# Kernel tuning notes

Measured on AMD Instinct MI355X. Metric: run time of the kernel, lower is better.

The kernel has to match this reference:

```python
import jax, jax.numpy as jnp
import numpy as np

REF_POSE = np.array([[213.33335876464844, 124.50563049316406], [190.504638671875, 115.11840057373047], [169.9791717529297, 101.77180480957031], [146.72341918945312, 96.25749206542969], [128.86770629882812, 87.2344970703125], [150.34292602539062, 101.61070251464844], [119.29926300048828, 98.73982238769531], [100.03463745117188, 99.74459838867188], [82.62400817871094, 101.2509536743164], [148.91049194335938, 112.71517181396484], [114.37303161621094, 113.20121002197266], [91.90096282958984, 116.49812316894531], [74.75020599365234, 119.37875366210938], [149.59658813476562, 124.09295654296875], [119.72419738769531, 126.36898040771484], [99.59107208251953, 129.40196228027344], [82.82524108886719, 131.584228515625], [154.55911254882812, 135.07681274414062], [133.8833770751953, 140.85983276367188], [120.45906066894531, 145.40306091308594], [106.21541595458984, 150.072265625]], dtype=np.float32)

SCALES = (0.25, 0.5, 1.0)
ORIENTATIONS = (0, 90, 180, 270)
INPUT_SIZE = (256, 256)          # (H, W)
ANCHOR_STRIDE = (1, 1)           # (y_stride, x_stride)
POS_TH = 0.5
KPT_SIGMA = 0.05                 # per-keypoint OKS falloff


def _generate_anchor_poses():
    # scale + rotate ref pose about its centroid -> [A, 21, 2]
    c = REF_POSE.mean(axis=0, keepdims=True)
    out = []
    for s in SCALES:
        for o in ORIENTATIONS:
            th = np.deg2rad(o)
            R = np.array([[np.cos(th), -np.sin(th)], [np.sin(th), np.cos(th)]], dtype=np.float32)
            out.append(c + s * (REF_POSE - c) @ R.T)
    return np.stack(out).astype(np.float32)


def _all_anchors(feat_h, feat_w):
    base = _generate_anchor_poses()                      # [A,21,2]
    w_ratio = INPUT_SIZE[1] / feat_w
    h_ratio = INPUT_SIZE[0] / feat_h
    sx = np.arange(0, feat_w, ANCHOR_STRIDE[1]) * w_ratio
    sy = np.arange(0, feat_h, ANCHOR_STRIDE[0]) * h_ratio
    gx, gy = np.meshgrid(sx, sy)
    shifts = np.stack([gx.ravel(), gy.ravel()], axis=1).astype(np.float32)  # [K,2]
    all_a = base[None, :, :, :] + shifts[:, None, None, :]                  # [K,A,21,2]
    return jnp.asarray(all_a.reshape(-1, 21, 2))                            # [K*A,21,2]


def _pose_oks(anchors, gt):
    # anchors [N,21,2], gt [B,2,21,3] -> OKS sim [B,N,2]
    d2 = jnp.sum((anchors[None, :, None, :, :] - gt[:, None, :, :, :2]) ** 2, axis=-1)  # [B,N,2,21]
    vis = (gt[..., 2] > 0).astype(anchors.dtype)[:, None, :, :]                          # [B,1,2,21]
    xy = gt[..., :2]
    area = jnp.prod(xy.max(axis=2) - xy.min(axis=2), axis=-1)                            # [B,2]
    s2 = jnp.maximum(area, 1.0)[:, None, :, None]                                        # [B,1,2,1]
    k2 = (2.0 * KPT_SIGMA) ** 2
    oks = jnp.exp(-d2 / (2.0 * s2 * k2))
    return jnp.sum(oks * vis, axis=-1) / jnp.maximum(jnp.sum(vis, axis=-1), 1.0)          # [B,N,2]


def setup_inputs() -> dict:
    key = jax.random.key(0)
    k1, k2 = jax.random.split(key)
    B = 16
    xy = jax.random.uniform(k1, (B, 42, 2), dtype=jnp.float32) * 216.0 + 20.0
    vis = jnp.ones((B, 42, 1), dtype=jnp.float32)
    pose_gt = jnp.concatenate([xy, vis], axis=-1)          # [B,42,3]
    hand_type = jnp.ones((B, 2), dtype=jnp.int32)          # both hands present
    return {"pose_gt": pose_gt, "hand_type": hand_type, "feat_h": 64, "feat_w": 64}


def reference(pose_gt, hand_type, feat_h, feat_w):
    all_anchors = _all_anchors(feat_h, feat_w)             # [N,21,2], N=K*A
    inside = jnp.sum((all_anchors[..., 0] >= 0) & (all_anchors[..., 1] >= 0)
                     & (all_anchors[..., 0] < INPUT_SIZE[0])
                     & (all_anchors[..., 1] < INPUT_SIZE[1]), axis=1) == 21  # [N]

    B = pose_gt.shape[0]
    gt = pose_gt.reshape(B, 2, 21, 3)                      # hand 0 = right, hand 1 = left
    sim = _pose_oks(all_anchors, gt)                       # [B,N,2]
    am = jnp.argmax(sim, axis=-1)                          # [B,N]
    mx = jnp.max(sim, axis=-1)                             # [B,N]

    right = (am == 0) & (mx > POS_TH) & (hand_type[:, 0:1] == 1) & inside[None, :]
    left = (am == 1) & (mx > POS_TH) & (hand_type[:, 1:2] == 1) & inside[None, :]
    neg = (~right) & (~left) & inside[None, :]

    # labels channel layout matches source: [:,:,0]=left, [:,:,1]=negative, [:,:,2]=right
    labels = jnp.stack([left, neg, right], axis=-1).astype(pose_gt.dtype)   # [B,N,3]
    labels = jnp.where(inside[None, :, None], labels, jnp.asarray(-1.0, pose_gt.dtype))

    pose_targets = (jnp.where(right[..., None, None], gt[:, 0][:, None], 0.0)
                    + jnp.where(left[..., None, None], gt[:, 1][:, None], 0.0))  # [B,N,21,3]

    offsets = pose_targets[..., :2] - all_anchors[None, :, :, :]             # [B,N,21,2]
    offsets = jnp.where(inside[None, :, None, None], offsets, 0.0)
    return all_anchors, inside, labels, offsets
```

## Files before the change

### kernel.cpp

```cpp
#include <hip/hip_runtime.h>
#include <math.h>

#define NA 49152
#define NB 16
#define ABLOCKS 192
#define EPS 1e-3f

__constant__ float RP[21][2] = {
  {213.33335876464844f, 124.50563049316406f},
  {190.504638671875f,   115.11840057373047f},
  {169.9791717529297f,  101.77180480957031f},
  {146.72341918945312f, 96.25749206542969f},
  {128.86770629882812f, 87.2344970703125f},
  {150.34292602539062f, 101.61070251464844f},
  {119.29926300048828f, 98.73982238769531f},
  {100.03463745117188f, 99.74459838867188f},
  {82.62400817871094f,  101.2509536743164f},
  {148.91049194335938f, 112.71517181396484f},
  {114.37303161621094f, 113.20121002197266f},
  {91.90096282958984f,  116.49812316894531f},
  {74.75020599365234f,  119.37875366210938f},
  {149.59658813476562f, 124.09295654296875f},
  {119.72419738769531f, 126.36898040771484f},
  {99.59107208251953f,  129.40196228027344f},
  {82.82524108886719f,  131.584228515625f},
  {154.55911254882812f, 135.07681274414062f},
  {133.8833770751953f,  140.85983276367188f},
  {120.45906066894531f, 145.40306091308594f},
  {106.21541595458984f, 150.072265625f}
};

__device__ __forceinline__ void ref_center(float& cx, float& cy) {
  #pragma clang fp contract(off)
  float rx[8], ry[8];
  #pragma unroll
  for (int j = 0; j < 8; ++j) {
    rx[j] = RP[j][0] + RP[j + 8][0];
    ry[j] = RP[j][1] + RP[j + 8][1];
  }
  float sx = ((rx[0] + rx[1]) + (rx[2] + rx[3])) + ((rx[4] + rx[5]) + (rx[6] + rx[7]));
  float sy = ((ry[0] + ry[1]) + (ry[2] + ry[3])) + ((ry[4] + ry[5]) + (ry[6] + ry[7]));
  #pragma unroll
  for (int j = 16; j < 21; ++j) { sx += RP[j][0]; sy += RP[j][1]; }
  cx = sx / 21.0f;
  cy = sy / 21.0f;
}

__device__ __forceinline__ float2 base_pt(int p, int j, float cx, float cy) {
  #pragma clang fp contract(off)
  const int si = p >> 2, oi = p & 3;
  const float s = (si == 0) ? 0.25f : (si == 1 ? 0.5f : 1.0f);
  const float dx = s * (RP[j][0] - cx);
  const float dy = s * (RP[j][1] - cy);
  const float rx = (oi == 0) ? dx : (oi == 1 ? -dy : (oi == 2 ? -dx : dy));
  const float ry = (oi == 0) ? dy : (oi == 1 ? dx : (oi == 2 ? -dy : -dx));
  return make_float2(cx + rx, cy + ry);
}

__device__ __forceinline__ void dec_anchor(int f2, int a0, const float2* sb2,
                                           float& anx, float& any,
                                           int& aloc, int& j) {
  #pragma clang fp contract(off)
  aloc = f2 / 21;
  j = f2 - aloc * 21;
  const int a = a0 + aloc;
  const int p = a % 12;
  const int kc = a / 12;
  const float shx = 4.0f * (float)(kc & 63);
  const float shy = 4.0f * (float)(kc >> 6);
  const float2 bpv = sb2[p * 21 + j];
  anx = bpv.x + shx;
  any = bpv.y + shy;
}

__device__ __forceinline__ float4 off_quad(int idx, int a0, const float2* sb2,
                                           const float* sgt, const int* shsel) {
  #pragma clang fp contract(off)
  float r[4];
  #pragma unroll
  for (int h = 0; h < 2; ++h) {
    float anx, any; int aloc, j;
    dec_anchor(idx * 2 + h, a0, sb2, anx, any, aloc, j);
    const int cc = shsel[aloc];
    const bool has = (cc == 1) || (cc == 2);
    const int hoff = (cc == 2) ? 63 : 0;
    const float tx = has ? sgt[hoff + j * 3] : 0.0f;
    const float ty = has ? sgt[hoff + j * 3 + 1] : 0.0f;
    r[h * 2]     = (cc >= 0) ? (tx - anx) : 0.0f;
    r[h * 2 + 1] = (cc >= 0) ? (ty - any) : 0.0f;
  }
  return make_float4(r[0], r[1], r[2], r[3]);
}

__device__ __forceinline__ float4 anc_quad(int idx, int a0, const float2* sb2) {
  float r[4];
  #pragma unroll
  for (int h = 0; h < 2; ++h) {
    float anx, any; int aloc, j;
    dec_anchor(idx * 2 + h, a0, sb2, anx, any, aloc, j);
    r[h * 2] = anx;
    r[h * 2 + 1] = any;
  }
  return make_float4(r[0], r[1], r[2], r[3]);
}

__global__ __launch_bounds__(256) void k_all(const float* __restrict__ gt,
                                             const int* __restrict__ ht,
                                             float* __restrict__ oa,
                                             float* __restrict__ oins,
                                             float* __restrict__ ol,
                                             float* __restrict__ oo) {
  __shared__ float2 sb2[252];
  __shared__ float sgt[126];
  __shared__ float sden[2], srden[2], snv[2];
  __shared__ int sht[2];
  __shared__ int shsel[256];
  __shared__ float sins[256];

  const int tid = threadIdx.x;
  const int b = blockIdx.x / ABLOCKS;
  const int ab = blockIdx.x % ABLOCKS;
  const int a0 = ab * 256;

  if (tid < 126) sgt[tid] = gt[b * 126 + tid];
  if (tid < 252) {
    float cx, cy; ref_center(cx, cy);
    const int p = tid / 21;
    const int j = tid - p * 21;
    sb2[tid] = base_pt(p, j, cx, cy);
  }
  if (tid == 252 || tid == 253) {
    const int h = tid - 252;
    const float* g = gt + b * 126 + h * 63;
    float mnx = g[0], mxx = g[0], mny = g[1], mxy = g[1];
    float nv = (g[2] > 0.0f) ? 1.0f : 0.0f;
    for (int j = 1; j < 21; ++j) {
      float x = g[j * 3], y = g[j * 3 + 1];
      mnx = fminf(mnx, x); mxx = fmaxf(mxx, x);
      mny = fminf(mny, y); mxy = fmaxf(mxy, y);
      nv += (g[j * 3 + 2] > 0.0f) ? 1.0f : 0.0f;
    }
    const float area = (mxx - mnx) * (mxy - mny);
    const float s2 = fmaxf(area, 1.0f);
    const float den = (2.0f * s2) * 0.01f;
    sden[h] = den;
    srden[h] = -1.0f / den;
    snv[h] = fmaxf(nv, 1.0f);
  }
  if (tid == 254 || tid == 255) sht[tid - 254] = ht[b * 2 + (tid - 254)];
  __syncthreads();

  const int a = a0 + tid;
  const int p = a % 12;
  const int kc = a / 12;
  const float shx = 4.0f * (float)(kc & 63);
  const float shy = 4.0f * (float)(kc >> 6);
  const float2* bp = sb2 + p * 21;

  const float rd0 = srden[0], rd1 = srden[1];
  bool inside = true;
  float s0f = 0.0f, s1f = 0.0f;
  #pragma unroll
  for (int j = 0; j < 21; ++j) {
    #pragma clang fp contract(off)
    const float anx = bp[j].x + shx;
    const float any = bp[j].y + shy;
    inside = inside && (anx >= 0.0f) && (any >= 0.0f) &&
                       (anx < 256.0f) && (any < 256.0f);
    const float dx0 = anx - sgt[j * 3],      dy0 = any - sgt[j * 3 + 1];
    const float dx1 = anx - sgt[63 + j * 3], dy1 = any - sgt[63 + j * 3 + 1];
    const float v0 = (sgt[j * 3 + 2] > 0.0f) ? 1.0f : 0.0f;
    const float v1 = (sgt[63 + j * 3 + 2] > 0.0f) ? 1.0f : 0.0f;
    s0f += __expf((dx0 * dx0 + dy0 * dy0) * rd0) * v0;
    s1f += __expf((dx1 * dx1 + dy1 * dy1) * rd1) * v1;
  }
  float sim0 = s0f / snv[0];
  float sim1 = s1f / snv[1];
  const float mxf = fmaxf(sim0, sim1);
  const bool need_exact = (fabsf(mxf - 0.5f) < EPS) ||
                          ((mxf > 0.5f - EPS) && (fabsf(sim0 - sim1) < EPS));

  if (need_exact) {
    #pragma clang fp contract(off)
    float q0[8], q1[8];
    #pragma unroll
    for (int j = 0; j < 16; ++j) {
      const float ax = bp[j].x + shx, ay = bp[j].y + shy;
      float dx0 = ax - sgt[j * 3], dy0 = ay - sgt[j * 3 + 1];
      float d20 = dx0 * dx0 + dy0 * dy0;
      float vv0 = (sgt[j * 3 + 2] > 0.0f) ? 1.0f : 0.0f;
      float t0 = (float)::exp((double)(-d20 / sden[0])) * vv0;
      float dx1 = ax - sgt[63 + j * 3], dy1 = ay - sgt[63 + j * 3 + 1];
      float d21 = dx1 * dx1 + dy1 * dy1;
      float vv1 = (sgt[63 + j * 3 + 2] > 0.0f) ? 1.0f : 0.0f;
      float t1 = (float)::exp((double)(-d21 / sden[1])) * vv1;
      if (j < 8) { q0[j] = t0; q1[j] = t1; }
      else       { q0[j - 8] += t0; q1[j - 8] += t1; }
    }
    float s0 = ((q0[0] + q0[1]) + (q0[2] + q0[3])) + ((q0[4] + q0[5]) + (q0[6] + q0[7]));
    float s1 = ((q1[0] + q1[1]) + (q1[2] + q1[3])) + ((q1[4] + q1[5]) + (q1[6] + q1[7]));
    #pragma unroll
    for (int j = 16; j < 21; ++j) {
      const float ax = bp[j].x + shx, ay = bp[j].y + shy;
      float dx0 = ax - sgt[j * 3], dy0 = ay - sgt[j * 3 + 1];
      float d20 = dx0 * dx0 + dy0 * dy0;
      float vv0 = (sgt[j * 3 + 2] > 0.0f) ? 1.0f : 0.0f;
      s0 += (float)::exp((double)(-d20 / sden[0])) * vv0;
      float dx1 = ax - sgt[63 + j * 3], dy1 = ay - sgt[63 + j * 3 + 1];
      float d21 = dx1 * dx1 + dy1 * dy1;
      float vv1 = (sgt[63 + j * 3 + 2] > 0.0f) ? 1.0f : 0.0f;
      s1 += (float)::exp((double)(-d21 / sden[1])) * vv1;
    }
    sim0 = s0 / snv[0];
    sim1 = s1 / snv[1];
  }

  const int am = (sim1 > sim0) ? 1 : 0;
  const float mx = fmaxf(sim0, sim1);
  const bool pos = mx > 0.5f;
  const bool right = (am == 0) && pos && (sht[0] == 1) && inside;
  const bool left  = (am == 1) && pos && (sht[1] == 1) && inside;

  int c;
  if (!inside)      c = -1;
  else if (right)   c = 1;
  else if (left)    c = 2;
  else              c = 0;
  shsel[tid] = c;
  sins[tid] = inside ? 1.0f : 0.0f;
  __syncthreads();

  if (tid < 192) {
    float4* lf4 = reinterpret_cast<float4*>(ol + ((size_t)b * NA + a0) * 3);
    float r[4];
    #pragma unroll
    for (int k = 0; k < 4; ++k) {
      const int q = tid * 4 + k;
      const int al = q / 3;
      const int rr = q - al * 3;
      const int cc = shsel[al];
      float v;
      if (cc < 0)       v = -1.0f;
      else if (rr == 0) v = (cc == 2) ? 1.0f : 0.0f;
      else if (rr == 1) v = (cc == 0) ? 1.0f : 0.0f;
      else              v = (cc == 1) ? 1.0f : 0.0f;
      r[k] = v;
    }
    lf4[tid] = make_float4(r[0], r[1], r[2], r[3]);
  }

  {
    float4* of4 = reinterpret_cast<float4*>(oo + ((size_t)b * NA + a0) * 42);
    #pragma unroll
    for (int i = 0; i < 10; ++i) {
      const int idx = i * 256 + tid;
      of4[idx] = off_quad(idx, a0, sb2, sgt, shsel);
    }
    if (tid < 128) {
      const int idx = 2560 + tid;
      of4[idx] = off_quad(idx, a0, sb2, sgt, shsel);
    }
  }

  if (b == 0) {
    float4* af4 = reinterpret_cast<float4*>(oa + (size_t)a0 * 42);
    #pragma unroll
    for (int i = 0; i < 10; ++i) {
      const int idx = i * 256 + tid;
      af4[idx] = anc_quad(idx, a0, sb2);
    }
    if (tid < 128) {
      const int idx = 2560 + tid;
      af4[idx] = anc_quad(idx, a0, sb2);
    }
    if (tid < 64) {
      float4* if4 = reinterpret_cast<float4*>(oins + a0);
      if4[tid] = make_float4(sins[tid * 4], sins[tid * 4 + 1],
                             sins[tid * 4 + 2], sins[tid * 4 + 3]);
    }
  }
}

extern "C" void kernel_launch(void* const* d_in, const int* in_sizes, int n_in,
                              void* d_out, int out_size, void* d_ws, size_t ws_size,
                              hipStream_t stream) {
  (void)in_sizes; (void)n_in; (void)d_ws; (void)ws_size; (void)out_size;
  const float* gt = (const float*)d_in[0];
  const int* ht = (const int*)d_in[1];
  float* out = (float*)d_out;
  float* out_anchors = out;
  float* out_inside  = out + (size_t)NA * 42;
  float* out_labels  = out + (size_t)NA * 43;
  float* out_offsets = out_labels + (size_t)NB * NA * 3;

  hipLaunchKernelGGL(k_all, dim3(NB * ABLOCKS), dim3(256), 0, stream,
                     gt, ht, out_anchors, out_inside, out_labels, out_offsets);
}
```

Baseline: 178.5 us.

## Split into decide and write kernels with nontemporal stores for outputs

The single fused kernel is split into two launches. The first computes OKS similarity and writes only the labels. The second reads the labels back to rebuild each anchor's class and writes the offsets, anchors and inside mask with nontemporal vector stores. The gt array is also repacked into xy/visibility shared arrays. The intent is to lighten register and LDS pressure in the write-heavy phase and stream its large output past the cache, at the cost of an extra launch and a reread of the labels.

```diff
diff --git a/kernel.cpp b/kernel.cpp
--- a/kernel.cpp
+++ b/kernel.cpp
@@ -5,6 +5,13 @@
 #define NB 16
 #define ABLOCKS 192
 #define EPS 1e-3f
+
+typedef __attribute__((ext_vector_type(4))) float f4v;
+
+__device__ __forceinline__ void nt_store4(float* p, float a, float b, float c, float d) {
+  f4v v; v.x = a; v.y = b; v.z = c; v.w = d;
+  __builtin_nontemporal_store(v, reinterpret_cast<f4v*>(p));
+}
 
 __constant__ float RP[21][2] = {
   {213.33335876464844f, 124.50563049316406f},
@@ -73,61 +80,30 @@
   any = bpv.y + shy;
 }
 
-__device__ __forceinline__ float4 off_quad(int idx, int a0, const float2* sb2,
-                                           const float* sgt, const int* shsel) {
-  #pragma clang fp contract(off)
-  float r[4];
-  #pragma unroll
-  for (int h = 0; h < 2; ++h) {
-    float anx, any; int aloc, j;
-    dec_anchor(idx * 2 + h, a0, sb2, anx, any, aloc, j);
-    const int cc = shsel[aloc];
-    const bool has = (cc == 1) || (cc == 2);
-    const int hoff = (cc == 2) ? 63 : 0;
-    const float tx = has ? sgt[hoff + j * 3] : 0.0f;
-    const float ty = has ? sgt[hoff + j * 3 + 1] : 0.0f;
-    r[h * 2]     = (cc >= 0) ? (tx - anx) : 0.0f;
-    r[h * 2 + 1] = (cc >= 0) ? (ty - any) : 0.0f;
-  }
-  return make_float4(r[0], r[1], r[2], r[3]);
-}
-
-__device__ __forceinline__ float4 anc_quad(int idx, int a0, const float2* sb2) {
-  float r[4];
-  #pragma unroll
-  for (int h = 0; h < 2; ++h) {
-    float anx, any; int aloc, j;
-    dec_anchor(idx * 2 + h, a0, sb2, anx, any, aloc, j);
-    r[h * 2] = anx;
-    r[h * 2 + 1] = any;
-  }
-  return make_float4(r[0], r[1], r[2], r[3]);
-}
-
-__global__ __launch_bounds__(256) void k_all(const float* __restrict__ gt,
-                                             const int* __restrict__ ht,
-                                             float* __restrict__ oa,
-                                             float* __restrict__ oins,
-                                             float* __restrict__ ol,
-                                             float* __restrict__ oo) {
+__global__ __launch_bounds__(256) void k_decide(const float* __restrict__ gt,
+                                                const int* __restrict__ ht,
+                                                float* __restrict__ ol) {
   __shared__ float2 sb2[252];
-  __shared__ float sgt[126];
+  __shared__ float2 sxy[42];
+  __shared__ float svis[42];
   __shared__ float sden[2], srden[2], snv[2];
   __shared__ int sht[2];
   __shared__ int shsel[256];
-  __shared__ float sins[256];
 
   const int tid = threadIdx.x;
   const int b = blockIdx.x / ABLOCKS;
   const int ab = blockIdx.x % ABLOCKS;
   const int a0 = ab * 256;
 
-  if (tid < 126) sgt[tid] = gt[b * 126 + tid];
   if (tid < 252) {
     float cx, cy; ref_center(cx, cy);
-    const int p = tid / 21;
-    const int j = tid - p * 21;
-    sb2[tid] = base_pt(p, j, cx, cy);
+    sb2[tid] = base_pt(tid / 21, tid % 21, cx, cy);
+  }
+  if (tid < 42) {
+    const int h = tid / 21, j = tid - h * 21;
+    const float* g = gt + b * 126 + h * 63 + j * 3;
+    sxy[tid] = make_float2(g[0], g[1]);
+    svis[tid] = g[2];
   }
   if (tid == 252 || tid == 253) {
     const int h = tid - 252;
@@ -167,10 +143,11 @@
     const float any = bp[j].y + shy;
     inside = inside && (anx >= 0.0f) && (any >= 0.0f) &&
                        (anx < 256.0f) && (any < 256.0f);
-    const float dx0 = anx - sgt[j * 3],      dy0 = any - sgt[j * 3 + 1];
-    const float dx1 = anx - sgt[63 + j * 3], dy1 = any - sgt[63 + j * 3 + 1];
-    const float v0 = (sgt[j * 3 + 2] > 0.0f) ? 1.0f : 0.0f;
-    const float v1 = (sgt[63 + j * 3 + 2] > 0.0f) ? 1.0f : 0.0f;
+    const float2 g0 = sxy[j], g1 = sxy[21 + j];
+    const float dx0 = anx - g0.x, dy0 = any - g0.y;
+    const float dx1 = anx - g1.x, dy1 = any - g1.y;
+    const float v0 = (svis[j] > 0.0f) ? 1.0f : 0.0f;
+    const float v1 = (svis[21 + j] > 0.0f) ? 1.0f : 0.0f;
     s0f += __expf((dx0 * dx0 + dy0 * dy0) * rd0) * v0;
     s1f += __expf((dx1 * dx1 + dy1 * dy1) * rd1) * v1;
   }
@@ -186,13 +163,14 @@
     #pragma unroll
     for (int j = 0; j < 16; ++j) {
       const float ax = bp[j].x + shx, ay = bp[j].y + shy;
-      float dx0 = ax - sgt[j * 3], dy0 = ay - sgt[j * 3 + 1];
+      const float2 g0 = sxy[j], g1 = sxy[21 + j];
+      float dx0 = ax - g0.x, dy0 = ay - g0.y;
       float d20 = dx0 * dx0 + dy0 * dy0;
-      float vv0 = (sgt[j * 3 + 2] > 0.0f) ? 1.0f : 0.0f;
+      float vv0 = (svis[j] > 0.0f) ? 1.0f : 0.0f;
       float t0 = (float)::exp((double)(-d20 / sden[0])) * vv0;
-      float dx1 = ax - sgt[63 + j * 3], dy1 = ay - sgt[63 + j * 3 + 1];
+      float dx1 = ax - g1.x, dy1 = ay - g1.y;
       float d21 = dx1 * dx1 + dy1 * dy1;
-      float vv1 = (sgt[63 + j * 3 + 2] > 0.0f) ? 1.0f : 0.0f;
+      float vv1 = (svis[21 + j] > 0.0f) ? 1.0f : 0.0f;
       float t1 = (float)::exp((double)(-d21 / sden[1])) * vv1;
       if (j < 8) { q0[j] = t0; q1[j] = t1; }
       else       { q0[j - 8] += t0; q1[j - 8] += t1; }
@@ -202,13 +180,14 @@
     #pragma unroll
     for (int j = 16; j < 21; ++j) {
       const float ax = bp[j].x + shx, ay = bp[j].y + shy;
-      float dx0 = ax - sgt[j * 3], dy0 = ay - sgt[j * 3 + 1];
+      const float2 g0 = sxy[j], g1 = sxy[21 + j];
+      float dx0 = ax - g0.x, dy0 = ay - g0.y;
       float d20 = dx0 * dx0 + dy0 * dy0;
-      float vv0 = (sgt[j * 3 + 2] > 0.0f) ? 1.0f : 0.0f;
+      float vv0 = (svis[j] > 0.0f) ? 1.0f : 0.0f;
       s0 += (float)::exp((double)(-d20 / sden[0])) * vv0;
-      float dx1 = ax - sgt[63 + j * 3], dy1 = ay - sgt[63 + j * 3 + 1];
+      float dx1 = ax - g1.x, dy1 = ay - g1.y;
       float d21 = dx1 * dx1 + dy1 * dy1;
-      float vv1 = (sgt[63 + j * 3 + 2] > 0.0f) ? 1.0f : 0.0f;
+      float vv1 = (svis[21 + j] > 0.0f) ? 1.0f : 0.0f;
       s1 += (float)::exp((double)(-d21 / sden[1])) * vv1;
     }
     sim0 = s0 / snv[0];
@@ -227,7 +206,6 @@
   else if (left)    c = 2;
   else              c = 0;
   shsel[tid] = c;
-  sins[tid] = inside ? 1.0f : 0.0f;
   __syncthreads();
 
   if (tid < 192) {
@@ -248,35 +226,95 @@
     }
     lf4[tid] = make_float4(r[0], r[1], r[2], r[3]);
   }
+}
+
+__global__ __launch_bounds__(256) void k_write(const float* __restrict__ gt,
+                                               const float* __restrict__ ol,
+                                               float* __restrict__ oa,
+                                               float* __restrict__ oins,
+                                               float* __restrict__ oo) {
+  __shared__ float2 sb2[252];
+  __shared__ float2 stg[42];
+  __shared__ int scc[256];
+
+  const int tid = threadIdx.x;
+  const int b = blockIdx.x / ABLOCKS;
+  const int ab = blockIdx.x % ABLOCKS;
+  const int a0 = ab * 256;
+
+  if (tid < 252) {
+    float cx, cy; ref_center(cx, cy);
+    sb2[tid] = base_pt(tid / 21, tid % 21, cx, cy);
+  }
+  if (tid < 42) {
+    const int h = tid / 21, j = tid - h * 21;
+    const float* g = gt + b * 126 + h * 63 + j * 3;
+    stg[tid] = make_float2(g[0], g[1]);
+  }
+  if (tid < 192) {
+    const float4 lv = reinterpret_cast<const float4*>(ol + ((size_t)b * NA + a0) * 3)[tid];
+    const float vv[4] = {lv.x, lv.y, lv.z, lv.w};
+    #pragma unroll
+    for (int k = 0; k < 4; ++k) {
+      const int q = tid * 4 + k;
+      const int al = q / 3;
+      const int rr = q - al * 3;
+      const float v = vv[k];
+      if (rr == 0 && v == -1.0f) scc[al] = 255;
+      else if (rr == 0 && v == 1.0f) scc[al] = 2;
+      else if (rr == 1 && v == 1.0f) scc[al] = 0;
+      else if (rr == 2 && v == 1.0f) scc[al] = 1;
+    }
+  }
+  __syncthreads();
 
   {
-    float4* of4 = reinterpret_cast<float4*>(oo + ((size_t)b * NA + a0) * 42);
-    #pragma unroll
-    for (int i = 0; i < 10; ++i) {
+    float* ob = oo + ((size_t)b * NA + a0) * 42;
+    #pragma unroll
+    for (int i = 0; i < 11; ++i) {
+      #pragma clang fp contract(off)
       const int idx = i * 256 + tid;
-      of4[idx] = off_quad(idx, a0, sb2, sgt, shsel);
-    }
-    if (tid < 128) {
-      const int idx = 2560 + tid;
-      of4[idx] = off_quad(idx, a0, sb2, sgt, shsel);
+      if (i == 10 && tid >= 128) break;
+      float r[4];
+      #pragma unroll
+      for (int h = 0; h < 2; ++h) {
+        float anx, any; int aloc, j;
+        dec_anchor(idx * 2 + h, a0, sb2, anx, any, aloc, j);
+        const int cc = scc[aloc];
+        const bool has = (cc == 1) || (cc == 2);
+        const int hoff = (cc == 2) ? 21 : 0;
+        const float tx = has ? stg[hoff + j].x : 0.0f;
+        const float ty = has ? stg[hoff + j].y : 0.0f;
+        r[h * 2]     = (cc != 255) ? (tx - anx) : 0.0f;
+        r[h * 2 + 1] = (cc != 255) ? (ty - any) : 0.0f;
+      }
+      nt_store4(ob + idx * 4, r[0], r[1], r[2], r[3]);
     }
   }
 
   if (b == 0) {
-    float4* af4 = reinterpret_cast<float4*>(oa + (size_t)a0 * 42);
-    #pragma unroll
-    for (int i = 0; i < 10; ++i) {
+    float* ab4 = oa + (size_t)a0 * 42;
+    #pragma unroll
+    for (int i = 0; i < 11; ++i) {
       const int idx = i * 256 + tid;
-      af4[idx] = anc_quad(idx, a0, sb2);
-    }
-    if (tid < 128) {
-      const int idx = 2560 + tid;
-      af4[idx] = anc_quad(idx, a0, sb2);
+      if (i == 10 && tid >= 128) break;
+      float r[4];
+      #pragma unroll
+      for (int h = 0; h < 2; ++h) {
+        float anx, any; int aloc, j;
+        dec_anchor(idx * 2 + h, a0, sb2, anx, any, aloc, j);
+        r[h * 2] = anx;
+        r[h * 2 + 1] = any;
+      }
+      nt_store4(ab4 + idx * 4, r[0], r[1], r[2], r[3]);
     }
     if (tid < 64) {
-      float4* if4 = reinterpret_cast<float4*>(oins + a0);
-      if4[tid] = make_float4(sins[tid * 4], sins[tid * 4 + 1],
-                             sins[tid * 4 + 2], sins[tid * 4 + 3]);
+      float* ib = oins + a0;
+      nt_store4(ib + tid * 4,
+                (scc[tid * 4]     != 255) ? 1.0f : 0.0f,
+                (scc[tid * 4 + 1] != 255) ? 1.0f : 0.0f,
+                (scc[tid * 4 + 2] != 255) ? 1.0f : 0.0f,
+                (scc[tid * 4 + 3] != 255) ? 1.0f : 0.0f);
     }
   }
 }
@@ -293,6 +331,8 @@
   float* out_labels  = out + (size_t)NA * 43;
   float* out_offsets = out_labels + (size_t)NB * NA * 3;
 
-  hipLaunchKernelGGL(k_all, dim3(NB * ABLOCKS), dim3(256), 0, stream,
-                     gt, ht, out_anchors, out_inside, out_labels, out_offsets);
-}
+  hipLaunchKernelGGL(k_decide, dim3(NB * ABLOCKS), dim3(256), 0, stream,
+                     gt, ht, out_labels);
+  hipLaunchKernelGGL(k_write, dim3(NB * ABLOCKS), dim3(256), 0, stream,
+                     gt, out_labels, out_anchors, out_inside, out_offsets);
+}
```

Result: slower. 192.8 us (+8.0%).

## Use nontemporal stores, precomputed anchor shifts, packed GT layout and incremental indexing

Applied to the files above, without the earlier changes.

Output stores become nontemporal vector stores, which bypass cache retention for the large streaming writes of offsets, labels and anchors. Per-anchor shift and base index are cached in shared memory, and the GT keypoints are repacked into float4/float2 pairs so each keypoint needs fewer LDS reads. The division and modulo by 21 in the output loops are replaced by incremental index stepping. A launch-bounds occupancy hint is also added, which may constrain register allocation.

```diff
diff --git a/kernel.cpp b/kernel.cpp
--- a/kernel.cpp
+++ b/kernel.cpp
@@ -5,6 +5,13 @@
 #define NB 16
 #define ABLOCKS 192
 #define EPS 1e-3f
+
+typedef __attribute__((ext_vector_type(4))) float f4v;
+
+__device__ __forceinline__ void nt_store4(float* p, float a, float b, float c, float d) {
+  f4v v; v.x = a; v.y = b; v.z = c; v.w = d;
+  __builtin_nontemporal_store(v, reinterpret_cast<f4v*>(p));
+}
 
 __constant__ float RP[21][2] = {
   {213.33335876464844f, 124.50563049316406f},
@@ -57,77 +64,35 @@
   return make_float2(cx + rx, cy + ry);
 }
 
-__device__ __forceinline__ void dec_anchor(int f2, int a0, const float2* sb2,
-                                           float& anx, float& any,
-                                           int& aloc, int& j) {
-  #pragma clang fp contract(off)
-  aloc = f2 / 21;
-  j = f2 - aloc * 21;
-  const int a = a0 + aloc;
-  const int p = a % 12;
-  const int kc = a / 12;
-  const float shx = 4.0f * (float)(kc & 63);
-  const float shy = 4.0f * (float)(kc >> 6);
-  const float2 bpv = sb2[p * 21 + j];
-  anx = bpv.x + shx;
-  any = bpv.y + shy;
-}
-
-__device__ __forceinline__ float4 off_quad(int idx, int a0, const float2* sb2,
-                                           const float* sgt, const int* shsel) {
-  #pragma clang fp contract(off)
-  float r[4];
-  #pragma unroll
-  for (int h = 0; h < 2; ++h) {
-    float anx, any; int aloc, j;
-    dec_anchor(idx * 2 + h, a0, sb2, anx, any, aloc, j);
-    const int cc = shsel[aloc];
-    const bool has = (cc == 1) || (cc == 2);
-    const int hoff = (cc == 2) ? 63 : 0;
-    const float tx = has ? sgt[hoff + j * 3] : 0.0f;
-    const float ty = has ? sgt[hoff + j * 3 + 1] : 0.0f;
-    r[h * 2]     = (cc >= 0) ? (tx - anx) : 0.0f;
-    r[h * 2 + 1] = (cc >= 0) ? (ty - any) : 0.0f;
-  }
-  return make_float4(r[0], r[1], r[2], r[3]);
-}
-
-__device__ __forceinline__ float4 anc_quad(int idx, int a0, const float2* sb2) {
-  float r[4];
-  #pragma unroll
-  for (int h = 0; h < 2; ++h) {
-    float anx, any; int aloc, j;
-    dec_anchor(idx * 2 + h, a0, sb2, anx, any, aloc, j);
-    r[h * 2] = anx;
-    r[h * 2 + 1] = any;
-  }
-  return make_float4(r[0], r[1], r[2], r[3]);
-}
-
-__global__ __launch_bounds__(256) void k_all(const float* __restrict__ gt,
-                                             const int* __restrict__ ht,
-                                             float* __restrict__ oa,
-                                             float* __restrict__ oins,
-                                             float* __restrict__ ol,
-                                             float* __restrict__ oo) {
+__global__ __launch_bounds__(256, 5) void k_all(const float* __restrict__ gt,
+                                                const int* __restrict__ ht,
+                                                float* __restrict__ oa,
+                                                float* __restrict__ oins,
+                                                float* __restrict__ ol,
+                                                float* __restrict__ oo) {
   __shared__ float2 sb2[252];
-  __shared__ float sgt[126];
+  __shared__ float4 sg4[21];
+  __shared__ float2 sv2[21];
   __shared__ float sden[2], srden[2], snv[2];
   __shared__ int sht[2];
-  __shared__ int shsel[256];
-  __shared__ float sins[256];
+  __shared__ float4 sanc[256];
+  __shared__ int scc[256];
 
   const int tid = threadIdx.x;
   const int b = blockIdx.x / ABLOCKS;
   const int ab = blockIdx.x % ABLOCKS;
   const int a0 = ab * 256;
 
-  if (tid < 126) sgt[tid] = gt[b * 126 + tid];
   if (tid < 252) {
     float cx, cy; ref_center(cx, cy);
-    const int p = tid / 21;
-    const int j = tid - p * 21;
-    sb2[tid] = base_pt(p, j, cx, cy);
+    sb2[tid] = base_pt(tid / 21, tid % 21, cx, cy);
+  }
+  if (tid < 21) {
+    const float* g0 = gt + b * 126 + tid * 3;
+    const float* g1 = g0 + 63;
+    sg4[tid] = make_float4(g0[0], g0[1], g1[0], g1[1]);
+    sv2[tid] = make_float2((g0[2] > 0.0f) ? 1.0f : 0.0f,
+                           (g1[2] > 0.0f) ? 1.0f : 0.0f);
   }
   if (tid == 252 || tid == 253) {
     const int h = tid - 252;
@@ -155,7 +120,8 @@
   const int kc = a / 12;
   const float shx = 4.0f * (float)(kc & 63);
   const float shy = 4.0f * (float)(kc >> 6);
-  const float2* bp = sb2 + p * 21;
+  const int pb = p * 21;
+  sanc[tid] = make_float4(shx, shy, (float)pb, 0.0f);
 
   const float rd0 = srden[0], rd1 = srden[1];
   bool inside = true;
@@ -163,16 +129,17 @@
   #pragma unroll
   for (int j = 0; j < 21; ++j) {
     #pragma clang fp contract(off)
-    const float anx = bp[j].x + shx;
-    const float any = bp[j].y + shy;
+    const float2 bpv = sb2[pb + j];
+    const float anx = bpv.x + shx;
+    const float any = bpv.y + shy;
     inside = inside && (anx >= 0.0f) && (any >= 0.0f) &&
                        (anx < 256.0f) && (any < 256.0f);
-    const float dx0 = anx - sgt[j * 3],      dy0 = any - sgt[j * 3 + 1];
-    const float dx1 = anx - sgt[63 + j * 3], dy1 = any - sgt[63 + j * 3 + 1];
-    const float v0 = (sgt[j * 3 + 2] > 0.0f) ? 1.0f : 0.0f;
-    const float v1 = (sgt[63 + j * 3 + 2] > 0.0f) ? 1.0f : 0.0f;
-    s0f += __expf((dx0 * dx0 + dy0 * dy0) * rd0) * v0;
-    s1f += __expf((dx1 * dx1 + dy1 * dy1) * rd1) * v1;
+    const float4 g = sg4[j];
+    const float2 v = sv2[j];
+    const float dx0 = anx - g.x, dy0 = any - g.y;
+    const float dx1 = anx - g.z, dy1 = any - g.w;
+    s0f += __expf((dx0 * dx0 + dy0 * dy0) * rd0) * v.x;
+    s1f += __expf((dx1 * dx1 + dy1 * dy1) * rd1) * v.y;
   }
   float sim0 = s0f / snv[0];
   float sim1 = s1f / snv[1];
@@ -180,20 +147,21 @@
   const bool need_exact = (fabsf(mxf - 0.5f) < EPS) ||
                           ((mxf > 0.5f - EPS) && (fabsf(sim0 - sim1) < EPS));
 
-  if (need_exact) {
+  if (__builtin_expect(need_exact, 0)) {
     #pragma clang fp contract(off)
     float q0[8], q1[8];
     #pragma unroll
     for (int j = 0; j < 16; ++j) {
-      const float ax = bp[j].x + shx, ay = bp[j].y + shy;
-      float dx0 = ax - sgt[j * 3], dy0 = ay - sgt[j * 3 + 1];
+      const float2 bpv = sb2[pb + j];
+      const float ax = bpv.x + shx, ay = bpv.y + shy;
+      const float4 g = sg4[j];
+      const float2 v = sv2[j];
+      float dx0 = ax - g.x, dy0 = ay - g.y;
       float d20 = dx0 * dx0 + dy0 * dy0;
-      float vv0 = (sgt[j * 3 + 2] > 0.0f) ? 1.0f : 0.0f;
-      float t0 = (float)::exp((double)(-d20 / sden[0])) * vv0;
-      float dx1 = ax - sgt[63 + j * 3], dy1 = ay - sgt[63 + j * 3 + 1];
+      float t0 = (float)::exp((double)(-d20 / sden[0])) * v.x;
+      float dx1 = ax - g.z, dy1 = ay - g.w;
       float d21 = dx1 * dx1 + dy1 * dy1;
-      float vv1 = (sgt[63 + j * 3 + 2] > 0.0f) ? 1.0f : 0.0f;
-      float t1 = (float)::exp((double)(-d21 / sden[1])) * vv1;
+      float t1 = (float)::exp((double)(-d21 / sden[1])) * v.y;
       if (j < 8) { q0[j] = t0; q1[j] = t1; }
       else       { q0[j - 8] += t0; q1[j - 8] += t1; }
     }
@@ -201,15 +169,16 @@
     float s1 = ((q1[0] + q1[1]) + (q1[2] + q1[3])) + ((q1[4] + q1[5]) + (q1[6] + q1[7]));
     #pragma unroll
     for (int j = 16; j < 21; ++j) {
-      const float ax = bp[j].x + shx, ay = bp[j].y + shy;
-      float dx0 = ax - sgt[j * 3], dy0 = ay - sgt[j * 3 + 1];
+      const float2 bpv = sb2[pb + j];
+      const float ax = bpv.x + shx, ay = bpv.y + shy;
+      const float4 g = sg4[j];
+      const float2 v = sv2[j];
+      float dx0 = ax - g.x, dy0 = ay - g.y;
       float d20 = dx0 * dx0 + dy0 * dy0;
-      float vv0 = (sgt[j * 3 + 2] > 0.0f) ? 1.0f : 0.0f;
-      s0 += (float)::exp((double)(-d20 / sden[0])) * vv0;
-      float dx1 = ax - sgt[63 + j * 3], dy1 = ay - sgt[63 + j * 3 + 1];
+      s0 += (float)::exp((double)(-d20 / sden[0])) * v.x;
+      float dx1 = ax - g.z, dy1 = ay - g.w;
       float d21 = dx1 * dx1 + dy1 * dy1;
-      float vv1 = (sgt[63 + j * 3 + 2] > 0.0f) ? 1.0f : 0.0f;
-      s1 += (float)::exp((double)(-d21 / sden[1])) * vv1;
+      s1 += (float)::exp((double)(-d21 / sden[1])) * v.y;
     }
     sim0 = s0 / snv[0];
     sim1 = s1 / snv[1];
@@ -226,19 +195,18 @@
   else if (right)   c = 1;
   else if (left)    c = 2;
   else              c = 0;
-  shsel[tid] = c;
-  sins[tid] = inside ? 1.0f : 0.0f;
+  scc[tid] = c;
   __syncthreads();
 
   if (tid < 192) {
-    float4* lf4 = reinterpret_cast<float4*>(ol + ((size_t)b * NA + a0) * 3);
+    float* lb = ol + ((size_t)b * NA + a0) * 3;
     float r[4];
     #pragma unroll
     for (int k = 0; k < 4; ++k) {
       const int q = tid * 4 + k;
       const int al = q / 3;
       const int rr = q - al * 3;
-      const int cc = shsel[al];
+      const int cc = scc[al];
       float v;
       if (cc < 0)       v = -1.0f;
       else if (rr == 0) v = (cc == 2) ? 1.0f : 0.0f;
@@ -246,37 +214,81 @@
       else              v = (cc == 1) ? 1.0f : 0.0f;
       r[k] = v;
     }
-    lf4[tid] = make_float4(r[0], r[1], r[2], r[3]);
+    nt_store4(lb + tid * 4, r[0], r[1], r[2], r[3]);
   }
 
   {
-    float4* of4 = reinterpret_cast<float4*>(oo + ((size_t)b * NA + a0) * 42);
-    #pragma unroll
-    for (int i = 0; i < 10; ++i) {
+    float* ob = oo + ((size_t)b * NA + a0) * 42;
+    int al = (2 * tid) / 21;
+    int jj = 2 * tid - al * 21;
+    #pragma unroll
+    for (int i = 0; i < 11; ++i) {
+      #pragma clang fp contract(off)
+      if (i == 10 && tid >= 128) break;
       const int idx = i * 256 + tid;
-      of4[idx] = off_quad(idx, a0, sb2, sgt, shsel);
-    }
-    if (tid < 128) {
-      const int idx = 2560 + tid;
-      of4[idx] = off_quad(idx, a0, sb2, sgt, shsel);
+      const bool w1 = (jj + 1) >= 21;
+      const int al1 = al + (w1 ? 1 : 0);
+      const int j1 = w1 ? 0 : (jj + 1);
+      float r[4];
+      {
+        const float4 sa = sanc[al];
+        const int cc = scc[al];
+        const float2 bpv = sb2[(int)sa.z + jj];
+        const float anx = bpv.x + sa.x, any = bpv.y + sa.y;
+        const float4 g = sg4[jj];
+        const bool has = (cc == 1) || (cc == 2);
+        float tx = (cc == 2) ? g.z : g.x;
+        float ty = (cc == 2) ? g.w : g.y;
+        tx = has ? tx : 0.0f; ty = has ? ty : 0.0f;
+        r[0] = (cc >= 0) ? (tx - anx) : 0.0f;
+        r[1] = (cc >= 0) ? (ty - any) : 0.0f;
+      }
+      {
+        const float4 sa = sanc[al1];
+        const int cc = scc[al1];
+        const float2 bpv = sb2[(int)sa.z + j1];
+        const float anx = bpv.x + sa.x, any = bpv.y + sa.y;
+        const float4 g = sg4[j1];
+        const bool has = (cc == 1) || (cc == 2);
+        float tx = (cc == 2) ? g.z : g.x;
+        float ty = (cc == 2) ? g.w : g.y;
+        tx = has ? tx : 0.0f; ty = has ? ty : 0.0f;
+        r[2] = (cc >= 0) ? (tx - anx) : 0.0f;
+        r[3] = (cc >= 0) ? (ty - any) : 0.0f;
+      }
+      nt_store4(ob + idx * 4, r[0], r[1], r[2], r[3]);
+      jj += 8; al += 24;
+      if (jj >= 21) { jj -= 21; ++al; }
     }
   }
 
   if (b == 0) {
-    float4* af4 = reinterpret_cast<float4*>(oa + (size_t)a0 * 42);
-    #pragma unroll
-    for (int i = 0; i < 10; ++i) {
+    float* ap = oa + (size_t)a0 * 42;
+    int al = (2 * tid) / 21;
+    int jj = 2 * tid - al * 21;
+    #pragma unroll
+    for (int i = 0; i < 11; ++i) {
+      if (i == 10 && tid >= 128) break;
       const int idx = i * 256 + tid;
-      af4[idx] = anc_quad(idx, a0, sb2);
-    }
-    if (tid < 128) {
-      const int idx = 2560 + tid;
-      af4[idx] = anc_quad(idx, a0, sb2);
+      const bool w1 = (jj + 1) >= 21;
+      const int al1 = al + (w1 ? 1 : 0);
+      const int j1 = w1 ? 0 : (jj + 1);
+      const float4 sa = sanc[al];
+      const float2 bpv = sb2[(int)sa.z + jj];
+      const float4 sb = sanc[al1];
+      const float2 bq = sb2[(int)sb.z + j1];
+      nt_store4(ap + idx * 4, bpv.x + sa.x, bpv.y + sa.y,
+                              bq.x + sb.x,  bq.y + sb.y);
+      jj += 8; al += 24;
+      if (jj >= 21) { jj -= 21; ++al; }
     }
     if (tid < 64) {
-      float4* if4 = reinterpret_cast<float4*>(oins + a0);
-      if4[tid] = make_float4(sins[tid * 4], sins[tid * 4 + 1],
-                             sins[tid * 4 + 2], sins[tid * 4 + 3]);
+      float* ib = oins + a0;
+      nt_store4(ib + tid * 4,
+                (scc[tid * 4]     >= 0) ? 1.0f : 0.0f,
+                (scc[tid * 4 + 1] >= 0) ? 1.0f : 0.0f,
+                (scc[tid * 4 + 2] >= 0) ? 1.0f : 0.0f,
+                (scc[tid * 4 + 3] >= 0) ? 1.0f : 0.0f);
     }
   }
 }
```

Result: faster. 164.5 us (-7.8%).
